# Optimization experiments

Hardware: AMD Instinct MI355X
Metric: run time of the kernel (lower is better)

## Reference

```python
import jax, jax.numpy as jnp
import numpy as np

A0 = 0.5291772105638411
KE = 14.399645351950548


def _softplus_inverse(x):
    return x + np.log(-np.expm1(-x))


def _sigma(x):
    # exp(-1/clamp(x,1e-12)) underflows to 0 for x<=0, so the where is nan-free
    return jnp.where(x > 0, jnp.exp(-1.0 / jnp.maximum(x, 1e-12)), 0.0)


def _switch(x, x_on, x_off):
    c = (x - x_on) / (x_off - x_on)
    s1 = _sigma(1.0 - c)
    s0 = _sigma(c)
    return s1 / (s1 + s0 + 1e-12)


def setup_inputs() -> dict:
    key = jax.random.key(0)
    k0, k1, k2, k3, k4 = jax.random.split(key, 5)
    N = 100000
    E = 6400000
    atomic_numbers = jax.random.uniform(k0, (N,), jnp.float32, 1.0, 30.0)
    cutoffs = jax.random.uniform(k1, (E, 1), jnp.float32)
    lengths = jax.random.uniform(k2, (E, 1), jnp.float32, 0.5, 3.0)
    senders = jax.random.randint(k3, (E,), 0, N)
    receivers = jax.random.randint(k4, (E,), 0, N)
    init = dict(a1=3.2, a2=0.9423, a3=0.4028, a4=0.2016,
                c1=0.1818, c2=0.5099, c3=0.2802, c4=0.02817,
                p=0.23, d=1.0 / (0.8854 * A0))
    params = {k + '_raw': jnp.asarray([_softplus_inverse(v)], jnp.float32)
              for k, v in init.items()}
    out = {'atomic_numbers': atomic_numbers, 'cutoffs': cutoffs,
           'senders': senders, 'receivers': receivers,
           'lengths': lengths, 'num_nodes': N}
    out.update(params)
    return out


def reference(atomic_numbers, cutoffs, senders, receivers, lengths, num_nodes,
              a1_raw, a2_raw, a3_raw, a4_raw,
              c1_raw, c2_raw, c3_raw, c4_raw, p_raw, d_raw):
    sp = jax.nn.softplus
    a1, a2, a3, a4 = sp(a1_raw), sp(a2_raw), sp(a3_raw), sp(a4_raw)
    c1, c2, c3, c4 = sp(c1_raw), sp(c2_raw), sp(c3_raw), sp(c4_raw)
    p, d = sp(p_raw), sp(d_raw)
    c_sum = c1 + c2 + c3 + c4
    c1, c2, c3, c4 = c1 / c_sum, c2 / c_sum, c3 / c_sum, c4 / c_sum

    cut = cutoffs[:, 0]   # [E]
    L = lengths[:, 0]     # [E]
    z_i = atomic_numbers[receivers]
    z_j = atomic_numbers[senders]

    x = KE * cut * (z_i * z_j) / jnp.maximum(L, 1e-6)
    rzd = L * (jnp.power(z_i, p) + jnp.power(z_j, p)) * d
    y = (c1 * jnp.exp(-a1 * rzd) + c2 * jnp.exp(-a2 * rzd)
         + c3 * jnp.exp(-a3 * rzd) + c4 * jnp.exp(-a4 * rzd))
    w = _switch(L, 0.0, 1.5)
    e_rep_edge = w * x * y * 0.5
    return jax.ops.segment_sum(e_rep_edge, receivers, num_segments=num_nodes)[:, None]
```

## Files before the change

kernel.cpp:

```cpp
#include <hip/hip_runtime.h>
#include <math.h>

#define C0KE 7.199822675975274f
#define LOG2E 1.4426950408889634f
#define BSHIFT 8
#define NBK 391
#define SLOTS 20
#define REG (NBK * SLOTS)
#define NBLK 512
#define K1T 512
#define SENTINEL 0xFFFFFFFFu

__device__ __forceinline__ float softplusf(float x) {
    return (x > 20.0f) ? x : log1pf(__expf(x));
}

struct ZblParams { float A1, A2, A3, A4, c1, c2, c3, c4, p; };

__device__ __forceinline__ void load_params(
    const float* a1r, const float* a2r, const float* a3r, const float* a4r,
    const float* c1r, const float* c2r, const float* c3r, const float* c4r,
    const float* pr, const float* dr, ZblParams* P)
{
    float d  = softplusf(dr[0]);
    float s  = d * LOG2E;
    P->A1 = softplusf(a1r[0]) * s;
    P->A2 = softplusf(a2r[0]) * s;
    P->A3 = softplusf(a3r[0]) * s;
    P->A4 = softplusf(a4r[0]) * s;
    float c1 = softplusf(c1r[0]), c2 = softplusf(c2r[0]);
    float c3 = softplusf(c3r[0]), c4 = softplusf(c4r[0]);
    float inv = 1.0f / (c1 + c2 + c3 + c4);
    P->c1 = c1 * inv; P->c2 = c2 * inv; P->c3 = c3 * inv; P->c4 = c4 * inv;
    P->p = softplusf(pr[0]);
}

__device__ __forceinline__ float edge_energy_fast(
    float l, float cut_, float zi, float zj, const ZblParams& P)
{
    float c  = l * (1.0f / 1.5f);
    float om = 1.0f - c;
    float s1 = __builtin_amdgcn_exp2f(-LOG2E * __builtin_amdgcn_rcpf(om));
    float s0 = __builtin_amdgcn_exp2f(-LOG2E * __builtin_amdgcn_rcpf(c));
    float w  = s1 * __builtin_amdgcn_rcpf(s1 + s0);
    float x  = C0KE * cut_ * zi * zj * __builtin_amdgcn_rcpf(l);
    float S  = __builtin_amdgcn_exp2f(P.p * __builtin_amdgcn_logf(zi))
             + __builtin_amdgcn_exp2f(P.p * __builtin_amdgcn_logf(zj));
    float t  = l * S;
    float y  = P.c1 * __builtin_amdgcn_exp2f(-P.A1 * t)
             + P.c2 * __builtin_amdgcn_exp2f(-P.A2 * t)
             + P.c3 * __builtin_amdgcn_exp2f(-P.A3 * t)
             + P.c4 * __builtin_amdgcn_exp2f(-P.A4 * t);
    return w * x * y;
}

__global__ __launch_bounds__(K1T) void zbl_build(
    const float* __restrict__ z, const float* __restrict__ cut,
    const int* __restrict__ snd, const int* __restrict__ rcv,
    const float* __restrict__ len,
    const float* __restrict__ a1r, const float* __restrict__ a2r,
    const float* __restrict__ a3r, const float* __restrict__ a4r,
    const float* __restrict__ c1r, const float* __restrict__ c2r,
    const float* __restrict__ c3r, const float* __restrict__ c4r,
    const float* __restrict__ pr,  const float* __restrict__ dr,
    unsigned* __restrict__ Pg,
    float* __restrict__ out,
    int EPB, int E)
{
    __shared__ ZblParams P;
    __shared__ unsigned slots[REG];
    __shared__ unsigned fillc[NBK];

    const int tid = threadIdx.x;
    if (tid == 0)
        load_params(a1r, a2r, a3r, a4r, c1r, c2r, c3r, c4r, pr, dr, &P);
    {
        uint4* s4p = (uint4*)slots;
        const uint4 sent = make_uint4(SENTINEL, SENTINEL, SENTINEL, SENTINEL);
        for (int i = tid; i < REG / 4; i += K1T) s4p[i] = sent;
    }
    for (int b = tid; b < NBK; b += K1T) fillc[b] = 0u;
    __syncthreads();
    const ZblParams Pl = P;

    const int blk = blockIdx.x;
    const int e0 = blk * EPB;
    const int e1 = min(e0 + EPB, E);
    const int nv = (e1 > e0) ? ((e1 - e0) >> 2) : 0;
    const int qb = e0 >> 2;
    const int etail = e0 + (nv << 2);
    const float4* Lq = (const float4*)len;
    const int4*   Rq = (const int4*)rcv;
    const float4* Cq = (const float4*)cut;
    const int4*   Sq = (const int4*)snd;

    const int trips = (nv + K1T - 1) / K1T;
    int rel = tid;
    int qi  = qb + tid;
    bool have = rel < nv;
    float4 l4, c4; int4 r4, s4;
    if (have) { l4 = Lq[qi]; r4 = Rq[qi]; c4 = Cq[qi]; s4 = Sq[qi]; }

    for (int it = 0; it < trips; ++it) {
        const int reln = rel + K1T;
        const int qin  = qi + K1T;
        const bool haveN = reln < nv;
        float4 l4n, c4n; int4 r4n, s4n;
        if (haveN) { l4n = Lq[qin]; r4n = Rq[qin]; c4n = Cq[qin]; s4n = Sq[qin]; }

        if (have) {
            float Ls[4] = {l4.x, l4.y, l4.z, l4.w};
            float Cs[4] = {c4.x, c4.y, c4.z, c4.w};
            int   Ss[4] = {s4.x, s4.y, s4.z, s4.w};
            int   Rs[4] = {r4.x, r4.y, r4.z, r4.w};
            bool  pass[4];
            float zi[4], zj[4];
            #pragma unroll
            for (int k = 0; k < 4; ++k) {
                pass[k] = Ls[k] < 1.5f;
                if (pass[k]) {
                    zi[k] = z[(unsigned)Rs[k]];
                    zj[k] = z[(unsigned)Ss[k]];
                }
            }
            #pragma unroll
            for (int k = 0; k < 4; ++k) {
                if (pass[k]) {
                    float v = edge_energy_fast(Ls[k], Cs[k], zi[k], zj[k], Pl);
                    unsigned r  = (unsigned)Rs[k];
                    unsigned bk = r >> BSHIFT;
                    unsigned tk = atomicAdd(&fillc[bk], 1u);
                    if (tk < SLOTS) {
                        slots[bk * SLOTS + tk] =
                            (__float_as_uint(v) & 0xFFFFFF00u) | (r & 0xFFu);
                    } else {
                        unsafeAtomicAdd(&out[r], v);
                    }
                }
            }
        }
        l4 = l4n; c4 = c4n; r4 = r4n; s4 = s4n;
        rel = reln; qi = qin; have = haveN;
    }

    for (int e = etail + tid; e < e1; e += K1T) {
        float l = len[e];
        if (l < 1.5f) {
            unsigned r = (unsigned)rcv[e];
            float v = edge_energy_fast(l, cut[e], z[r], z[(unsigned)snd[e]], Pl);
            unsigned bk = r >> BSHIFT;
            unsigned tk = atomicAdd(&fillc[bk], 1u);
            if (tk < SLOTS)
                slots[bk * SLOTS + tk] =
                    (__float_as_uint(v) & 0xFFFFFF00u) | (r & 0xFFu);
            else
                unsafeAtomicAdd(&out[r], v);
        }
    }
    __syncthreads();

    {
        uint4* dst = (uint4*)(Pg + (size_t)blk * REG);
        const uint4* src = (const uint4*)slots;
        for (int i = tid; i < REG / 4; i += K1T) dst[i] = src[i];
    }
}

__global__ __launch_bounds__(512) void zbl_reduce(
    const unsigned* __restrict__ Pg, float* __restrict__ out, int N)
{
    __shared__ float acc[256];
    const int tid = threadIdx.x;
    if (tid < 256) acc[tid] = 0.0f;
    __syncthreads();

    const int b = blockIdx.x;
    const uint4* Pq = (const uint4*)Pg;
    const int total = NBLK * (SLOTS / 4);
    for (int lin = tid; lin < total; lin += 512) {
        int r = lin / (SLOTS / 4);
        int q = lin - r * (SLOTS / 4);
        uint4 u = Pq[(size_t)r * (REG / 4) + (size_t)b * (SLOTS / 4) + q];
        if (u.x != SENTINEL)
            atomicAdd(&acc[u.x & 255u], __uint_as_float(u.x & 0xFFFFFF00u));
        if (u.y != SENTINEL)
            atomicAdd(&acc[u.y & 255u], __uint_as_float(u.y & 0xFFFFFF00u));
        if (u.z != SENTINEL)
            atomicAdd(&acc[u.z & 255u], __uint_as_float(u.z & 0xFFFFFF00u));
        if (u.w != SENTINEL)
            atomicAdd(&acc[u.w & 255u], __uint_as_float(u.w & 0xFFFFFF00u));
    }
    __syncthreads();

    int n = (b << BSHIFT) + tid;
    if (tid < 256 && n < N)
        out[n] += acc[tid];
}

__global__ __launch_bounds__(256) void zbl_direct(
    const float* __restrict__ z, const float* __restrict__ cut,
    const int* __restrict__ snd, const int* __restrict__ rcv,
    const float* __restrict__ len,
    const float* __restrict__ a1r, const float* __restrict__ a2r,
    const float* __restrict__ a3r, const float* __restrict__ a4r,
    const float* __restrict__ c1r, const float* __restrict__ c2r,
    const float* __restrict__ c3r, const float* __restrict__ c4r,
    const float* __restrict__ pr,  const float* __restrict__ dr,
    float* __restrict__ out, int n4, int E)
{
    __shared__ ZblParams P;
    if (threadIdx.x == 0)
        load_params(a1r, a2r, a3r, a4r, c1r, c2r, c3r, c4r, pr, dr, &P);
    __syncthreads();
    const ZblParams Pl = P;

    int i = blockIdx.x * blockDim.x + threadIdx.x;
    if (i >= n4) return;
    int base = i * 4;
    float cs[4], Ls[4]; int ss[4], rr[4]; int cnt;
    if (base + 4 <= E) {
        float4 c4v = ((const float4*)cut)[i];
        float4 l4v = ((const float4*)len)[i];
        int4   s4v = ((const int4*)snd)[i];
        int4   r4v = ((const int4*)rcv)[i];
        cs[0]=c4v.x; cs[1]=c4v.y; cs[2]=c4v.z; cs[3]=c4v.w;
        Ls[0]=l4v.x; Ls[1]=l4v.y; Ls[2]=l4v.z; Ls[3]=l4v.w;
        ss[0]=s4v.x; ss[1]=s4v.y; ss[2]=s4v.z; ss[3]=s4v.w;
        rr[0]=r4v.x; rr[1]=r4v.y; rr[2]=r4v.z; rr[3]=r4v.w;
        cnt = 4;
    } else {
        cnt = E - base;
        for (int k = 0; k < cnt; ++k) {
            cs[k] = cut[base+k]; Ls[k] = len[base+k];
            ss[k] = snd[base+k]; rr[k] = rcv[base+k];
        }
    }
    #pragma unroll
    for (int k = 0; k < 4; ++k) {
        if (k >= cnt) break;
        if (Ls[k] < 1.5f) {
            float e_rep = edge_energy_fast(Ls[k], cs[k], z[rr[k]], z[ss[k]], Pl);
            unsafeAtomicAdd(&out[rr[k]], e_rep);
        }
    }
}

extern "C" void kernel_launch(void* const* d_in, const int* in_sizes, int n_in,
                              void* d_out, int out_size, void* d_ws, size_t ws_size,
                              hipStream_t stream) {
    const float* z   = (const float*)d_in[0];
    const float* cut = (const float*)d_in[1];
    const int*   snd = (const int*)d_in[2];
    const int*   rcv = (const int*)d_in[3];
    const float* len = (const float*)d_in[4];
    const float* a1r = (const float*)d_in[6];
    const float* a2r = (const float*)d_in[7];
    const float* a3r = (const float*)d_in[8];
    const float* a4r = (const float*)d_in[9];
    const float* c1r = (const float*)d_in[10];
    const float* c2r = (const float*)d_in[11];
    const float* c3r = (const float*)d_in[12];
    const float* c4r = (const float*)d_in[13];
    const float* pr  = (const float*)d_in[14];
    const float* dr  = (const float*)d_in[15];

    float* out = (float*)d_out;
    int E = in_sizes[2];
    int N = out_size;

    size_t need1 = (size_t)NBLK * REG * sizeof(unsigned);

    hipMemsetAsync(d_out, 0, (size_t)N * sizeof(float), stream);

    if (ws_size >= need1) {
        int EPB = (((E + NBLK - 1) / NBLK) + 3) & ~3;
        unsigned* Pg = (unsigned*)d_ws;
        hipLaunchKernelGGL(zbl_build, dim3(NBLK), dim3(K1T), 0, stream,
                           z, cut, snd, rcv, len,
                           a1r, a2r, a3r, a4r, c1r, c2r, c3r, c4r, pr, dr,
                           Pg, out, EPB, E);
        hipLaunchKernelGGL(zbl_reduce, dim3(NBK), dim3(512), 0, stream,
                           (const unsigned*)Pg, out, N);
    } else {
        int n4 = (E + 3) / 4;
        int blocks = (n4 + 255) / 256;
        hipLaunchKernelGGL(zbl_direct, dim3(blocks), dim3(256), 0, stream,
                           z, cut, snd, rcv, len,
                           a1r, a2r, a3r, a4r, c1r, c2r, c3r, c4r, pr, dr,
                           out, n4, E);
    }
}
```

Measured before the change: 198.2 us.

## Fuse build and reduce into one cooperative kernel with bucket-major scratch layout

```diff
diff --git a/kernel.cpp b/kernel.cpp
--- a/kernel.cpp
+++ b/kernel.cpp
@@ -1,5 +1,8 @@
 #include <hip/hip_runtime.h>
+#include <hip/hip_cooperative_groups.h>
 #include <math.h>
+
+namespace cg = cooperative_groups;
 
 #define C0KE 7.199822675975274f
 #define LOG2E 1.4426950408889634f
@@ -9,6 +12,7 @@
 #define REG (NBK * SLOTS)
 #define NBLK 512
 #define K1T 512
+#define BCH (NBLK * SLOTS / 4)
 #define SENTINEL 0xFFFFFFFFu
 
 __device__ __forceinline__ float softplusf(float x) {
@@ -54,36 +58,14 @@
     return w * x * y;
 }
 
-__global__ __launch_bounds__(K1T) void zbl_build(
+__device__ __forceinline__ void phaseA(
     const float* __restrict__ z, const float* __restrict__ cut,
     const int* __restrict__ snd, const int* __restrict__ rcv,
-    const float* __restrict__ len,
-    const float* __restrict__ a1r, const float* __restrict__ a2r,
-    const float* __restrict__ a3r, const float* __restrict__ a4r,
-    const float* __restrict__ c1r, const float* __restrict__ c2r,
-    const float* __restrict__ c3r, const float* __restrict__ c4r,
-    const float* __restrict__ pr,  const float* __restrict__ dr,
-    unsigned* __restrict__ Pg,
-    float* __restrict__ out,
-    int EPB, int E)
-{
-    __shared__ ZblParams P;
-    __shared__ unsigned slots[REG];
-    __shared__ unsigned fillc[NBK];
-
-    const int tid = threadIdx.x;
-    if (tid == 0)
-        load_params(a1r, a2r, a3r, a4r, c1r, c2r, c3r, c4r, pr, dr, &P);
-    {
-        uint4* s4p = (uint4*)slots;
-        const uint4 sent = make_uint4(SENTINEL, SENTINEL, SENTINEL, SENTINEL);
-        for (int i = tid; i < REG / 4; i += K1T) s4p[i] = sent;
-    }
-    for (int b = tid; b < NBK; b += K1T) fillc[b] = 0u;
-    __syncthreads();
-    const ZblParams Pl = P;
-
-    const int blk = blockIdx.x;
+    const float* __restrict__ len, const ZblParams& Pl,
+    unsigned* slots, unsigned* fillc,
+    unsigned* __restrict__ Pg, float* __restrict__ out,
+    int EPB, int E, int blk, int tid)
+{
     const int e0 = blk * EPB;
     const int e1 = min(e0 + EPB, E);
     const int nv = (e1 > e0) ? ((e1 - e0) >> 2) : 0;
@@ -160,27 +142,26 @@
     __syncthreads();
 
     {
-        uint4* dst = (uint4*)(Pg + (size_t)blk * REG);
+        uint4* dst = (uint4*)Pg;
         const uint4* src = (const uint4*)slots;
-        for (int i = tid; i < REG / 4; i += K1T) dst[i] = src[i];
-    }
-}
-
-__global__ __launch_bounds__(512) void zbl_reduce(
-    const unsigned* __restrict__ Pg, float* __restrict__ out, int N)
-{
-    __shared__ float acc[256];
-    const int tid = threadIdx.x;
+        for (int c = tid; c < REG / 4; c += K1T) {
+            int bk = c / (SLOTS / 4);
+            int q  = c - bk * (SLOTS / 4);
+            dst[(size_t)bk * BCH + (size_t)blk * (SLOTS / 4) + q] = src[c];
+        }
+    }
+}
+
+__device__ __forceinline__ void phaseB(
+    const unsigned* __restrict__ Pg, float* acc,
+    float* __restrict__ out, int N, int b, int tid)
+{
     if (tid < 256) acc[tid] = 0.0f;
     __syncthreads();
 
-    const int b = blockIdx.x;
-    const uint4* Pq = (const uint4*)Pg;
-    const int total = NBLK * (SLOTS / 4);
-    for (int lin = tid; lin < total; lin += 512) {
-        int r = lin / (SLOTS / 4);
-        int q = lin - r * (SLOTS / 4);
-        uint4 u = Pq[(size_t)r * (REG / 4) + (size_t)b * (SLOTS / 4) + q];
+    const uint4* Pq = (const uint4*)Pg + (size_t)b * BCH;
+    for (int lin = tid; lin < BCH; lin += K1T) {
+        uint4 u = Pq[lin];
         if (u.x != SENTINEL)
             atomicAdd(&acc[u.x & 255u], __uint_as_float(u.x & 0xFFFFFF00u));
         if (u.y != SENTINEL)
@@ -195,6 +176,84 @@
     int n = (b << BSHIFT) + tid;
     if (tid < 256 && n < N)
         out[n] += acc[tid];
+}
+
+__global__ __launch_bounds__(K1T) void zbl_fused(
+    const float* __restrict__ z, const float* __restrict__ cut,
+    const int* __restrict__ snd, const int* __restrict__ rcv,
+    const float* __restrict__ len,
+    const float* __restrict__ a1r, const float* __restrict__ a2r,
+    const float* __restrict__ a3r, const float* __restrict__ a4r,
+    const float* __restrict__ c1r, const float* __restrict__ c2r,
+    const float* __restrict__ c3r, const float* __restrict__ c4r,
+    const float* __restrict__ pr,  const float* __restrict__ dr,
+    unsigned* __restrict__ Pg, float* __restrict__ out,
+    int EPB, int E, int N)
+{
+    __shared__ ZblParams P;
+    __shared__ unsigned slots[REG];
+    __shared__ unsigned fillc[NBK];
+    __shared__ float acc[256];
+
+    const int tid = threadIdx.x;
+    const int blk = blockIdx.x;
+    if (tid == 0)
+        load_params(a1r, a2r, a3r, a4r, c1r, c2r, c3r, c4r, pr, dr, &P);
+    {
+        uint4* s4p = (uint4*)slots;
+        const uint4 sent = make_uint4(SENTINEL, SENTINEL, SENTINEL, SENTINEL);
+        for (int i = tid; i < REG / 4; i += K1T) s4p[i] = sent;
+    }
+    for (int b = tid; b < NBK; b += K1T) fillc[b] = 0u;
+    __syncthreads();
+    const ZblParams Pl = P;
+
+    phaseA(z, cut, snd, rcv, len, Pl, slots, fillc, Pg, out, EPB, E, blk, tid);
+
+    __threadfence();
+    cg::this_grid().sync();
+
+    if (blk < NBK)
+        phaseB(Pg, acc, out, N, blk, tid);
+}
+
+__global__ __launch_bounds__(K1T) void zbl_build_bm(
+    const float* __restrict__ z, const float* __restrict__ cut,
+    const int* __restrict__ snd, const int* __restrict__ rcv,
+    const float* __restrict__ len,
+    const float* __restrict__ a1r, const float* __restrict__ a2r,
+    const float* __restrict__ a3r, const float* __restrict__ a4r,
+    const float* __restrict__ c1r, const float* __restrict__ c2r,
+    const float* __restrict__ c3r, const float* __restrict__ c4r,
+    const float* __restrict__ pr,  const float* __restrict__ dr,
+    unsigned* __restrict__ Pg, float* __restrict__ out,
+    int EPB, int E)
+{
+    __shared__ ZblParams P;
+    __shared__ unsigned slots[REG];
+    __shared__ unsigned fillc[NBK];
+
+    const int tid = threadIdx.x;
+    const int blk = blockIdx.x;
+    if (tid == 0)
+        load_params(a1r, a2r, a3r, a4r, c1r, c2r, c3r, c4r, pr, dr, &P);
+    {
+        uint4* s4p = (uint4*)slots;
+        const uint4 sent = make_uint4(SENTINEL, SENTINEL, SENTINEL, SENTINEL);
+        for (int i = tid; i < REG / 4; i += K1T) s4p[i] = sent;
+    }
+    for (int b = tid; b < NBK; b += K1T) fillc[b] = 0u;
+    __syncthreads();
+    const ZblParams Pl = P;
+
+    phaseA(z, cut, snd, rcv, len, Pl, slots, fillc, Pg, out, EPB, E, blk, tid);
+}
+
+__global__ __launch_bounds__(K1T) void zbl_reduce_bm(
+    const unsigned* __restrict__ Pg, float* __restrict__ out, int N)
+{
+    __shared__ float acc[256];
+    phaseB(Pg, acc, out, N, blockIdx.x, threadIdx.x);
 }
 
 __global__ __launch_bounds__(256) void zbl_direct(
@@ -275,12 +334,25 @@
     if (ws_size >= need1) {
         int EPB = (((E + NBLK - 1) / NBLK) + 3) & ~3;
         unsigned* Pg = (unsigned*)d_ws;
-        hipLaunchKernelGGL(zbl_build, dim3(NBLK), dim3(K1T), 0, stream,
-                           z, cut, snd, rcv, len,
-                           a1r, a2r, a3r, a4r, c1r, c2r, c3r, c4r, pr, dr,
-                           Pg, out, EPB, E);
-        hipLaunchKernelGGL(zbl_reduce, dim3(NBK), dim3(512), 0, stream,
-                           (const unsigned*)Pg, out, N);
+
+        void* args[] = {
+            (void*)&z,   (void*)&cut, (void*)&snd, (void*)&rcv, (void*)&len,
+            (void*)&a1r, (void*)&a2r, (void*)&a3r, (void*)&a4r,
+            (void*)&c1r, (void*)&c2r, (void*)&c3r, (void*)&c4r,
+            (void*)&pr,  (void*)&dr,
+            (void*)&Pg,  (void*)&out, (void*)&EPB, (void*)&E, (void*)&N
+        };
+        hipError_t err = hipLaunchCooperativeKernel(
+            (const void*)zbl_fused, dim3(NBLK), dim3(K1T), args, 0, stream);
+
+        if (err != hipSuccess) {
+            hipLaunchKernelGGL(zbl_build_bm, dim3(NBLK), dim3(K1T), 0, stream,
+                               z, cut, snd, rcv, len,
+                               a1r, a2r, a3r, a4r, c1r, c2r, c3r, c4r, pr, dr,
+                               Pg, out, EPB, E);
+            hipLaunchKernelGGL(zbl_reduce_bm, dim3(NBK), dim3(K1T), 0, stream,
+                               (const unsigned*)Pg, out, N);
+        }
     } else {
         int n4 = (E + 3) / 4;
         int blocks = (n4 + 255) / 256;
```

Result: slower. 422.8 us (+113.3%).
